# Kernel optimization log

Hardware: AMD Instinct MI355X
Metric: run time of the kernel (lower is better)

## Reference

```python
import jax, jax.numpy as jnp
import numpy as np


def setup_inputs() -> dict:
    key = jax.random.key(0)
    ks = jax.random.split(key, 6)
    B, U, O, S = 4096, 256, 128, 48
    scale_k = 1.0 / np.sqrt(O)
    scale_r = 1.0 / np.sqrt(U)
    return {
        "last_input": jax.random.normal(ks[0], (B, O), dtype=jnp.float32),
        "h0": jnp.zeros((B, U), dtype=jnp.float32),
        "c0": jnp.zeros((B, U), dtype=jnp.float32),
        "kernel": jax.random.normal(ks[1], (O, 4 * U), dtype=jnp.float32) * scale_k,
        "rec_kernel": jax.random.normal(ks[2], (U, 4 * U), dtype=jnp.float32) * scale_r,
        "bias": jax.random.normal(ks[3], (4 * U,), dtype=jnp.float32) * 0.1,
        "dense_w": jax.random.normal(ks[4], (U, O), dtype=jnp.float32) * scale_r,
        "dense_b": jax.random.normal(ks[5], (O,), dtype=jnp.float32) * 0.1,
        "output_steps": S,
    }


def _lstm_step(x, h, c, kernel, rec_kernel, bias):
    # Keras LSTMCell gate order: i, f, g (candidate), o
    z = x @ kernel + h @ rec_kernel + bias  # [B, 4U]
    i, f, g, o = jnp.split(z, 4, axis=-1)
    c_new = jax.nn.sigmoid(f) * c + jax.nn.sigmoid(i) * jnp.tanh(g)
    h_new = jax.nn.sigmoid(o) * jnp.tanh(c_new)
    return h_new, c_new


def reference(last_input, h0, c0, kernel, rec_kernel, bias, dense_w, dense_b, output_steps):
    def step(carry, _):
        x, h, c = carry
        h, c = _lstm_step(x, h, c, kernel, rec_kernel, bias)
        y = jax.nn.relu(h @ dense_w + dense_b)  # [B, O]
        return (y, h, c), y

    (_, _, _), ys = jax.lax.scan(step, (last_input, h0, c0), None, length=output_steps)
    # ys: [S, B, O] -> [B, S, O]
    return jnp.transpose(ys, (1, 0, 2))
```

## Files before the change

kernel.cpp:

```cpp
#include <hip/hip_runtime.h>
#include <hip/hip_bf16.h>

#define UDIM    256
#define ODIM    128
#define ZDIM    1024
#define NSTEPS  48
#define BM      16
#define THREADS 1024
#define NBLOCKS 256

#define KR_FRAGS 393216
#define D_FRAGS  32768

#define SA_W 392

typedef _Float16 f16x8 __attribute__((ext_vector_type(8)));
typedef float    f32x4 __attribute__((ext_vector_type(4)));

__device__ __forceinline__ ushort f2h_bits(float v) {
    _Float16 h = (_Float16)v;
    return *reinterpret_cast<ushort*>(&h);
}
__device__ __forceinline__ float sigmoid_f(float x) {
    return 1.0f / (1.0f + __expf(-x));
}
__device__ __forceinline__ float tanh_f(float x) {
    return 1.0f - 2.0f / (__expf(2.0f * x) + 1.0f);
}

__global__ void prep_weights(const float* __restrict__ kernel_w,
                             const float* __restrict__ rec_w,
                             const float* __restrict__ dense_w,
                             ushort* __restrict__ ws) {
    int idx = blockIdx.x * blockDim.x + threadIdx.x;
    if (idx < KR_FRAGS) {
        int j  = idx & 7;
        int l  = (idx >> 3) & 63;
        int fc = idx >> 9;
        int kc = fc % 12;
        int n  = fc / 12;
        int k   = kc * 32 + (l >> 4) * 8 + j;
        int col = n * 16 + (l & 15);
        float wv = (k < 128) ? kernel_w[k * ZDIM + col]
                             : rec_w[(k - 128) * ZDIM + col];
        ws[idx] = f2h_bits(wv);
    } else if (idx < KR_FRAGS + D_FRAGS) {
        int e  = idx - KR_FRAGS;
        int j  = e & 7;
        int l  = (e >> 3) & 63;
        int kc = (e >> 9) & 7;
        int n  = e >> 12;
        int k   = kc * 32 + (l >> 4) * 8 + j;
        int col = n * 16 + (l & 15);
        ws[KR_FRAGS + e] = f2h_bits(dense_w[k * ODIM + col]);
    }
}

__global__ __launch_bounds__(THREADS, 4) void lstm_mfma_kernel(
    const float* __restrict__ last_input,
    const float* __restrict__ h0,
    const float* __restrict__ c0,
    const float* __restrict__ bias,
    const float* __restrict__ dense_b,
    const ushort* __restrict__ wsro,
    float* __restrict__ out)
{
    const ushort* KR = wsro;

    __shared__ ushort sA[BM][SA_W];
    __shared__ __align__(16) ushort sDw[D_FRAGS];

    const int t  = threadIdx.x;
    const int w  = t >> 6;
    const int l  = t & 63;
    const int cl = l & 15;
    const int rg = l >> 4;
    const int blockRow = blockIdx.x * BM;

    for (int i = t * 8; i < D_FRAGS; i += THREADS * 8)
        *reinterpret_cast<f16x8*>(&sDw[i]) =
            *reinterpret_cast<const f16x8*>(&wsro[KR_FRAGS + i]);

    for (int i = t; i < BM * ODIM; i += THREADS) {
        int r = i >> 7, c = i & 127;
        sA[r][c] = f2h_bits(last_input[(blockRow + r) * ODIM + c]);
    }
    for (int i = t; i < BM * UDIM; i += THREADS) {
        int r = i >> 8, c = i & 255;
        sA[r][128 + c] = f2h_bits(h0[(blockRow + r) * UDIM + c]);
    }

    const int unit = 16 * w + cl;
    float cstate[4];
    #pragma unroll
    for (int r = 0; r < 4; ++r)
        cstate[r] = c0[(blockRow + 4 * rg + r) * UDIM + unit];

    float bz[4];
    #pragma unroll
    for (int g = 0; g < 4; ++g)
        bz[g] = bias[256 * g + unit];
    const float db = dense_b[16 * (w & 7) + cl];

    __syncthreads();

    for (int s = 0; s < NSTEPS; ++s) {
        f32x4 acc[4];
        #pragma unroll
        for (int g = 0; g < 4; ++g)
            acc[g] = (f32x4){bz[g], bz[g], bz[g], bz[g]};

        #pragma unroll 4
        for (int kc = 0; kc < 12; ++kc) {
            const int koff = kc * 32 + rg * 8;
            f16x8 a = *reinterpret_cast<const f16x8*>(&sA[cl][koff]);
            #pragma unroll
            for (int g = 0; g < 4; ++g) {
                const int n = w + 16 * g;
                const int fo = ((n * 12 + kc) * 64 + l) * 8;
                f16x8 b = *reinterpret_cast<const f16x8*>(KR + fo);
                acc[g] = __builtin_amdgcn_mfma_f32_16x16x32_f16(a, b, acc[g], 0, 0, 0);
            }
        }
        __syncthreads();

        #pragma unroll
        for (int r = 0; r < 4; ++r) {
            float iv = sigmoid_f(acc[0][r]);
            float fv = sigmoid_f(acc[1][r]);
            float gv = tanh_f(acc[2][r]);
            float ov = sigmoid_f(acc[3][r]);
            float cn = fv * cstate[r] + iv * gv;
            cstate[r] = cn;
            float hv = ov * tanh_f(cn);
            sA[4 * rg + r][128 + unit] = f2h_bits(hv);
        }
        __syncthreads();

        if (w < 8) {
            f32x4 dacc = (f32x4){db, db, db, db};
            #pragma unroll
            for (int kc = 0; kc < 8; ++kc) {
                const int koff = 128 + kc * 32 + rg * 8;
                f16x8 ah = *reinterpret_cast<const f16x8*>(&sA[cl][koff]);
                f16x8 b  = *reinterpret_cast<const f16x8*>(&sDw[w * 4096 + kc * 512 + l * 8]);
                dacc = __builtin_amdgcn_mfma_f32_16x16x32_f16(ah, b, dacc, 0, 0, 0);
            }
            #pragma unroll
            for (int r = 0; r < 4; ++r) {
                float y = fmaxf(dacc[r], 0.0f);
                int row = 4 * rg + r;
                out[((size_t)(blockRow + row) * NSTEPS + s) * ODIM + 16 * w + cl] = y;
                sA[row][16 * w + cl] = f2h_bits(y);
            }
        }
        __syncthreads();
    }
}

extern "C" void kernel_launch(void* const* d_in, const int* in_sizes, int n_in,
                              void* d_out, int out_size, void* d_ws, size_t ws_size,
                              hipStream_t stream) {
    const float* last_input = (const float*)d_in[0];
    const float* h0         = (const float*)d_in[1];
    const float* c0         = (const float*)d_in[2];
    const float* kernel_w   = (const float*)d_in[3];
    const float* rec_w      = (const float*)d_in[4];
    const float* bias       = (const float*)d_in[5];
    const float* dense_w    = (const float*)d_in[6];
    const float* dense_b    = (const float*)d_in[7];
    float* out  = (float*)d_out;
    ushort* ws  = (ushort*)d_ws;

    const int prep_total = KR_FRAGS + D_FRAGS;
    hipLaunchKernelGGL(prep_weights, dim3((prep_total + 255) / 256), dim3(256), 0, stream,
                       kernel_w, rec_w, dense_w, ws);
    hipLaunchKernelGGL(lstm_mfma_kernel, dim3(NBLOCKS), dim3(THREADS), 0, stream,
                       last_input, h0, c0, bias, dense_b, (const ushort*)ws, out);
}
```

Before: 420.8 us.

## Double-buffer h and overlap next-step recurrent GEMM with dense layer

Splits the gate GEMM into its recurrent part (h @ rec_kernel) and its input part (y @ kernel). The recurrent part for step s+1 is computed right after h is written, alongside the dense-layer MFMAs, so the next step only has to do the small input part after y is ready. The hidden state is ping-ponged between two shared-memory buffers, which removes one barrier per step and lets waves 8-15 do useful work while waves 0-7 run the dense layer. The cost is a larger shared-memory tile and extra accumulator registers, which may reduce occupancy.

```diff
diff --git a/kernel.cpp b/kernel.cpp
--- a/kernel.cpp
+++ b/kernel.cpp
@@ -12,7 +12,7 @@
 #define KR_FRAGS 393216
 #define D_FRAGS  32768
 
-#define SA_W 392
+#define SA_W 648
 
 typedef _Float16 f16x8 __attribute__((ext_vector_type(8)));
 typedef float    f32x4 __attribute__((ext_vector_type(4)));
@@ -87,7 +87,7 @@
     }
     for (int i = t; i < BM * UDIM; i += THREADS) {
         int r = i >> 8, c = i & 255;
-        sA[r][128 + c] = f2h_bits(h0[(blockRow + r) * UDIM + c]);
+        sA[r][384 + c] = f2h_bits(h0[(blockRow + r) * UDIM + c]);
     }
 
     const int unit = 16 * w + cl;
@@ -104,14 +104,29 @@
 
     __syncthreads();
 
+    f32x4 acc[4];
+    #pragma unroll
+    for (int g = 0; g < 4; ++g)
+        acc[g] = (f32x4){bz[g], bz[g], bz[g], bz[g]};
+
+    #pragma unroll 4
+    for (int kc = 4; kc < 12; ++kc) {
+        const int koff = 384 + (kc - 4) * 32 + rg * 8;
+        f16x8 a = *reinterpret_cast<const f16x8*>(&sA[cl][koff]);
+        #pragma unroll
+        for (int g = 0; g < 4; ++g) {
+            const int n = w + 16 * g;
+            const int fo = ((n * 12 + kc) * 64 + l) * 8;
+            f16x8 b = *reinterpret_cast<const f16x8*>(KR + fo);
+            acc[g] = __builtin_amdgcn_mfma_f32_16x16x32_f16(a, b, acc[g], 0, 0, 0);
+        }
+    }
+
     for (int s = 0; s < NSTEPS; ++s) {
-        f32x4 acc[4];
-        #pragma unroll
-        for (int g = 0; g < 4; ++g)
-            acc[g] = (f32x4){bz[g], bz[g], bz[g], bz[g]};
+        const int hb = 128 + 256 * (s & 1);
 
         #pragma unroll 4
-        for (int kc = 0; kc < 12; ++kc) {
+        for (int kc = 0; kc < 4; ++kc) {
             const int koff = kc * 32 + rg * 8;
             f16x8 a = *reinterpret_cast<const f16x8*>(&sA[cl][koff]);
             #pragma unroll
@@ -122,7 +137,6 @@
                 acc[g] = __builtin_amdgcn_mfma_f32_16x16x32_f16(a, b, acc[g], 0, 0, 0);
             }
         }
-        __syncthreads();
 
         #pragma unroll
         for (int r = 0; r < 4; ++r) {
@@ -133,15 +147,35 @@
             float cn = fv * cstate[r] + iv * gv;
             cstate[r] = cn;
             float hv = ov * tanh_f(cn);
-            sA[4 * rg + r][128 + unit] = f2h_bits(hv);
+            sA[4 * rg + r][hb + unit] = f2h_bits(hv);
         }
         __syncthreads();
+
+        f32x4 acc2[4];
+        #pragma unroll
+        for (int g = 0; g < 4; ++g)
+            acc2[g] = (f32x4){bz[g], bz[g], bz[g], bz[g]};
+
+        if (s < NSTEPS - 1) {
+            #pragma unroll 4
+            for (int kc = 4; kc < 12; ++kc) {
+                const int koff = hb + (kc - 4) * 32 + rg * 8;
+                f16x8 a = *reinterpret_cast<const f16x8*>(&sA[cl][koff]);
+                #pragma unroll
+                for (int g = 0; g < 4; ++g) {
+                    const int n = w + 16 * g;
+                    const int fo = ((n * 12 + kc) * 64 + l) * 8;
+                    f16x8 b = *reinterpret_cast<const f16x8*>(KR + fo);
+                    acc2[g] = __builtin_amdgcn_mfma_f32_16x16x32_f16(a, b, acc2[g], 0, 0, 0);
+                }
+            }
+        }
 
         if (w < 8) {
             f32x4 dacc = (f32x4){db, db, db, db};
             #pragma unroll
             for (int kc = 0; kc < 8; ++kc) {
-                const int koff = 128 + kc * 32 + rg * 8;
+                const int koff = hb + kc * 32 + rg * 8;
                 f16x8 ah = *reinterpret_cast<const f16x8*>(&sA[cl][koff]);
                 f16x8 b  = *reinterpret_cast<const f16x8*>(&sDw[w * 4096 + kc * 512 + l * 8]);
                 dacc = __builtin_amdgcn_mfma_f32_16x16x32_f16(ah, b, dacc, 0, 0, 0);
@@ -155,6 +189,10 @@
             }
         }
         __syncthreads();
+
+        #pragma unroll
+        for (int g = 0; g < 4; ++g)
+            acc[g] = acc2[g];
     }
 }
 
```

Result: faster. 361.9 us (-14.0%).

## Double batch tile per block, double-buffer hidden state, drop a barrier

Applied to the files above, without the earlier changes.

Each block now handles 32 batch rows instead of 16, so every weight fragment loaded from global memory feeds two MFMAs. This halves the weight traffic per row in the recurrent GEMM. The hidden state is ping-ponged between two shared-memory buffers, which removes one __syncthreads per step, and all 16 waves now take part in the dense projection. The cost is half as many blocks (128 on a chip with more CUs), more registers for the doubled accumulators, and larger shared memory, which may reduce occupancy.

```diff
diff --git a/kernel.cpp b/kernel.cpp
--- a/kernel.cpp
+++ b/kernel.cpp
@@ -5,14 +5,14 @@
 #define ODIM    128
 #define ZDIM    1024
 #define NSTEPS  48
-#define BM      16
+#define BM      32
 #define THREADS 1024
-#define NBLOCKS 256
+#define NBLOCKS 128
 
 #define KR_FRAGS 393216
 #define D_FRAGS  32768
 
-#define SA_W 392
+#define SA_W 648
 
 typedef _Float16 f16x8 __attribute__((ext_vector_type(8)));
 typedef float    f32x4 __attribute__((ext_vector_type(4)));
@@ -87,71 +87,86 @@
     }
     for (int i = t; i < BM * UDIM; i += THREADS) {
         int r = i >> 8, c = i & 255;
-        sA[r][128 + c] = f2h_bits(h0[(blockRow + r) * UDIM + c]);
+        sA[r][384 + c] = f2h_bits(h0[(blockRow + r) * UDIM + c]);
     }
 
     const int unit = 16 * w + cl;
-    float cstate[4];
+    float cstate[2][4];
     #pragma unroll
-    for (int r = 0; r < 4; ++r)
-        cstate[r] = c0[(blockRow + 4 * rg + r) * UDIM + unit];
+    for (int rt = 0; rt < 2; ++rt)
+        #pragma unroll
+        for (int r = 0; r < 4; ++r)
+            cstate[rt][r] = c0[(blockRow + rt * 16 + 4 * rg + r) * UDIM + unit];
 
     float bz[4];
     #pragma unroll
     for (int g = 0; g < 4; ++g)
         bz[g] = bias[256 * g + unit];
-    const float db = dense_b[16 * (w & 7) + cl];
+
+    const int dn  = w & 7;
+    const int drt = w >> 3;
+    const float db = dense_b[16 * dn + cl];
 
     __syncthreads();
 
     for (int s = 0; s < NSTEPS; ++s) {
-        f32x4 acc[4];
+        const int hrd = 128 + 256 * ((s + 1) & 1);
+        const int hb  = 128 + 256 * (s & 1);
+
+        f32x4 acc[4][2];
         #pragma unroll
-        for (int g = 0; g < 4; ++g)
-            acc[g] = (f32x4){bz[g], bz[g], bz[g], bz[g]};
+        for (int g = 0; g < 4; ++g) {
+            acc[g][0] = (f32x4){bz[g], bz[g], bz[g], bz[g]};
+            acc[g][1] = (f32x4){bz[g], bz[g], bz[g], bz[g]};
+        }
 
         #pragma unroll 4
         for (int kc = 0; kc < 12; ++kc) {
-            const int koff = kc * 32 + rg * 8;
-            f16x8 a = *reinterpret_cast<const f16x8*>(&sA[cl][koff]);
+            const int koff = (kc < 4) ? (kc * 32 + rg * 8)
+                                      : (hrd + (kc - 4) * 32 + rg * 8);
+            f16x8 a0 = *reinterpret_cast<const f16x8*>(&sA[cl][koff]);
+            f16x8 a1 = *reinterpret_cast<const f16x8*>(&sA[16 + cl][koff]);
             #pragma unroll
             for (int g = 0; g < 4; ++g) {
                 const int n = w + 16 * g;
                 const int fo = ((n * 12 + kc) * 64 + l) * 8;
                 f16x8 b = *reinterpret_cast<const f16x8*>(KR + fo);
-                acc[g] = __builtin_amdgcn_mfma_f32_16x16x32_f16(a, b, acc[g], 0, 0, 0);
+                acc[g][0] = __builtin_amdgcn_mfma_f32_16x16x32_f16(a0, b, acc[g][0], 0, 0, 0);
+                acc[g][1] = __builtin_amdgcn_mfma_f32_16x16x32_f16(a1, b, acc[g][1], 0, 0, 0);
+            }
+        }
+
+        #pragma unroll
+        for (int rt = 0; rt < 2; ++rt) {
+            #pragma unroll
+            for (int r = 0; r < 4; ++r) {
+                float iv = sigmoid_f(acc[0][rt][r]);
+                float fv = sigmoid_f(acc[1][rt][r]);
+                float gv = tanh_f(acc[2][rt][r]);
+                float ov = sigmoid_f(acc[3][rt][r]);
+                float cn = fv * cstate[rt][r] + iv * gv;
+                cstate[rt][r] = cn;
+                float hv = ov * tanh_f(cn);
+                sA[rt * 16 + 4 * rg + r][hb + unit] = f2h_bits(hv);
             }
         }
         __syncthreads();
 
-        #pragma unroll
-        for (int r = 0; r < 4; ++r) {
-            float iv = sigmoid_f(acc[0][r]);
-            float fv = sigmoid_f(acc[1][r]);
-            float gv = tanh_f(acc[2][r]);
-            float ov = sigmoid_f(acc[3][r]);
-            float cn = fv * cstate[r] + iv * gv;
-            cstate[r] = cn;
-            float hv = ov * tanh_f(cn);
-            sA[4 * rg + r][128 + unit] = f2h_bits(hv);
-        }
-        __syncthreads();
-
-        if (w < 8) {
+        {
             f32x4 dacc = (f32x4){db, db, db, db};
             #pragma unroll
             for (int kc = 0; kc < 8; ++kc) {
-                const int koff = 128 + kc * 32 + rg * 8;
-                f16x8 ah = *reinterpret_cast<const f16x8*>(&sA[cl][koff]);
-                f16x8 b  = *reinterpret_cast<const f16x8*>(&sDw[w * 4096 + kc * 512 + l * 8]);
+                const int koff = hb + kc * 32 + rg * 8;
+                f16x8 ah = *reinterpret_cast<const f16x8*>(&sA[drt * 16 + cl][koff]);
+                f16x8 b  = *reinterpret_cast<const f16x8*>(&sDw[dn * 4096 + kc * 512 + l * 8]);
                 dacc = __builtin_amdgcn_mfma_f32_16x16x32_f16(ah, b, dacc, 0, 0, 0);
             }
             #pragma unroll
             for (int r = 0; r < 4; ++r) {
                 float y = fmaxf(dacc[r], 0.0f);
-                int row = 4 * rg + r;
-                out[((size_t)(blockRow + row) * NSTEPS + s) * ODIM + 16 * w + cl] = y;
-                sA[row][16 * w + cl] = f2h_bits(y);
+                int row = drt * 16 + 4 * rg + r;
+                out[((size_t)(blockRow + row) * NSTEPS + s) * ODIM + 16 * dn + cl] = y;
+                sA[row][16 * dn + cl] = f2h_bits(y);
             }
         }
         __syncthreads();
```

New measurement: 507.2 us. 20.5% more time.
